# Kernel optimization log

Hardware: AMD Instinct MI355X
Metric: run time of the kernel (lower is better)

The kernel has to match this reference:

```python
import jax, jax.numpy as jnp
import numpy as np
import math

D, DK, DV = 1024, 128, 128
B, S = 4, 2048

def setup_inputs() -> dict:
    key = jax.random.key(0)
    k1, k2, k3, k4 = jax.random.split(key, 4)
    # xavier_normal std = sqrt(2/(fan_in+fan_out))
    std_qk = math.sqrt(2.0 / (D + DK))
    std_v = math.sqrt(2.0 / (D + DV))
    return {
        "X": jax.random.normal(k1, (B, S, D), dtype=jnp.float32),
        "W_q": jax.random.normal(k2, (D, DK), dtype=jnp.float32) * std_qk,
        "W_k": jax.random.normal(k3, (D, DK), dtype=jnp.float32) * std_qk,
        "W_v": jax.random.normal(k4, (D, DV), dtype=jnp.float32) * std_v,
    }

def reference(X, W_q, W_k, W_v):
    # Q,K,V projections: [B,S,D] @ [D,dk] -> [B,S,dk]
    Q = X @ W_q
    K = X @ W_k
    V = X @ W_v
    scale = 1.0 / math.sqrt(DK)
    # NOTE: original torch code calls A.masked_fill(...) without assigning the
    # result, so the causal mask is never actually applied. We replicate the
    # executed math: unmasked scaled dot-product attention.
    A = jnp.einsum("bqd,bkd->bqk", Q, K) * scale  # [B,S,S]
    A = jax.nn.softmax(A, axis=2)
    return jnp.einsum("bqk,bkv->bqv", A, V)  # [B,S,DV]
```

## Files before the change

kernel.cpp:

```cpp
#include <hip/hip_runtime.h>
#include <stdint.h>
#include <math.h>


typedef __attribute__((ext_vector_type(4))) float  f32x4;
typedef __attribute__((ext_vector_type(4))) short  s16x4;
typedef __attribute__((ext_vector_type(8))) short  s16x8;
typedef __attribute__((ext_vector_type(4))) float  fl4;

#define MFMA16(a,b,c) __builtin_amdgcn_mfma_f32_16x16x16bf16_1k(a,b,c,0,0,0)
#define MFMA32(a,b,c) __builtin_amdgcn_mfma_f32_16x16x32_bf16(a,b,c,0,0,0)

__device__ __forceinline__ short f2bf(float f){
  uint32_t u = __builtin_bit_cast(uint32_t, f);
  u = (u + 0x7FFFu + ((u >> 16) & 1u)) >> 16;
  return (short)u;
}

#define S_LEN   2048
#define D_IN    1024
#define D_HEAD  128
#define NROWS   8192
#define NSPLIT  8
#define KVB     64
#define KVPER   (S_LEN / NSPLIT)
#define NT      (KVPER / KVB)
#define QBLK    128

#define WT_OFF  0u
#define Q_OFF   786432u
#define K_OFF   (786432u + 2097152u)
#define V_OFF   (786432u + 2u*2097152u)
#define OP_OFF  (786432u + 3u*2097152u)
#define ML_OFF  (OP_OFF + 33554432u)

#define LOG2E   1.4426950408889634f
#define DEFER_TH 11.541560327111708f

__global__ __launch_bounds__(256) void wt3_kernel(
    const float* __restrict__ Wq, const float* __restrict__ Wk,
    const float* __restrict__ Wv, short* __restrict__ Wt){
  int i = blockIdx.x * 256 + threadIdx.x;
  int m = i >> 17;
  int r = i & 131071;
  int n = r >> 10;
  int k = r & 1023;
  const float* W = (m == 0) ? Wq : (m == 1 ? Wk : Wv);
  float v = W[k * D_HEAD + n];
  if (m == 0) v *= 0.08838834764831845f * LOG2E;
  Wt[i] = f2bf(v);
}

__global__ __launch_bounds__(256) void proj_kernel(
    const float* __restrict__ X, const short* __restrict__ Wt,
    short* __restrict__ Qo, short* __restrict__ Ko, short* __restrict__ Vt){
  const int mt  = blockIdx.x;
  const int mat = blockIdx.y;
  const short* Wm = Wt + mat * 131072;

  __shared__ short Xs[64][72];
  __shared__ short Ws[128][72];

  const int tid  = threadIdx.x;
  const int lane = tid & 63;
  const int wid  = tid >> 6;
  const int wm   = (wid >> 1) * 32;
  const int wn   = (wid & 1) * 64;
  const int lr   = lane & 15;
  const int lg8  = (lane >> 4) * 8;

  const f32x4 zero4 = {0.f, 0.f, 0.f, 0.f};
  f32x4 acc[2][4];
  #pragma unroll
  for (int mf = 0; mf < 2; mf++)
    #pragma unroll
    for (int n = 0; n < 4; n++) acc[mf][n] = zero4;

  const int xr = tid >> 2, xc = (tid & 3) * 16;
  const int wr = tid >> 1, wc = (tid & 1) * 32;

  const float* xsrc0 = X + (size_t)(mt * 64 + xr) * D_IN + xc;
  const short* wsrc0 = Wm + (size_t)wr * D_IN + wc;

  fl4   xA[4];
  s16x8 wR[4];

  #pragma unroll
  for (int j = 0; j < 4; j++){
    xA[j] = *(const fl4*)(xsrc0 + 4 * j);
    wR[j] = *(const s16x8*)(wsrc0 + 8 * j);
  }

  #pragma unroll 1
  for (int kt = 0; kt < D_IN; kt += 64){
    {
      s16x8 v0, v1;
      #pragma unroll
      for (int j = 0; j < 4; j++){
        v0[j] = f2bf(xA[0][j]); v0[j+4] = f2bf(xA[1][j]);
        v1[j] = f2bf(xA[2][j]); v1[j+4] = f2bf(xA[3][j]);
      }
      *(s16x8*)&Xs[xr][xc]     = v0;
      *(s16x8*)&Xs[xr][xc + 8] = v1;
      #pragma unroll
      for (int j = 0; j < 4; j++) *(s16x8*)&Ws[wr][wc + 8*j] = wR[j];
    }
    __syncthreads();

    if (kt + 64 < D_IN){
      #pragma unroll
      for (int j = 0; j < 4; j++){
        xA[j] = *(const fl4*)(xsrc0 + kt + 64 + 4*j);
        wR[j] = *(const s16x8*)(wsrc0 + kt + 64 + 8*j);
      }
    }

    #pragma unroll
    for (int kc = 0; kc < 64; kc += 32){
      s16x8 af[2];
      #pragma unroll
      for (int mf = 0; mf < 2; mf++)
        af[mf] = *(const s16x8*)&Xs[wm + mf*16 + lr][kc + lg8];
      #pragma unroll
      for (int n = 0; n < 4; n++){
        s16x8 bf = *(const s16x8*)&Ws[wn + n*16 + lr][kc + lg8];
        #pragma unroll
        for (int mf = 0; mf < 2; mf++)
          acc[mf][n] = MFMA32(af[mf], bf, acc[mf][n]);
      }
    }
    __syncthreads();
  }

  const int lg4 = (lane >> 4) * 4;
  if (mat < 2){
    short* dst = (mat == 0) ? Qo : Ko;
    #pragma unroll
    for (int mf = 0; mf < 2; mf++)
      #pragma unroll
      for (int n = 0; n < 4; n++){
        int col = wn + n*16 + lr;
        #pragma unroll
        for (int r = 0; r < 4; r++){
          int row = mt*64 + wm + mf*16 + lg4 + r;
          dst[(size_t)row * D_HEAD + col] = f2bf(acc[mf][n][r]);
        }
      }
  } else {
    const int b  = (mt * 64) >> 11;
    const int s0 = (mt * 64) & 2047;
    #pragma unroll
    for (int mf = 0; mf < 2; mf++)
      #pragma unroll
      for (int n = 0; n < 4; n++){
        int dv = wn + n*16 + lr;
        int s  = s0 + wm + mf*16 + lg4;
        s16x4 v;
        #pragma unroll
        for (int r = 0; r < 4; r++) v[r] = f2bf(acc[mf][n][r]);
        *(s16x4*)&Vt[((size_t)b * D_HEAD + dv) * S_LEN + s] = v;
      }
  }
}

__global__ __launch_bounds__(256) void flash_kernel(
    const short* __restrict__ Q, const short* __restrict__ K,
    const short* __restrict__ Vt, float* __restrict__ Opart,
    float* __restrict__ MLpart){
  const int sp = blockIdx.x;
  const int qt = blockIdx.y;
  const int b  = blockIdx.z;

  __shared__ short Ks[KVB][136];
  __shared__ short Vs[128][72];

  const int tid  = threadIdx.x;
  const int lane = tid & 63;
  const int w    = tid >> 6;
  const int lr   = lane & 15;
  const int lg   = lane >> 4;

  const int qrow0 = qt * QBLK + w * 32 + lr;
  const short* Qr = Q + (size_t)(b * S_LEN + qrow0) * D_HEAD + 8 * lg;
  s16x8 qf[2][4];
  #pragma unroll
  for (int qi = 0; qi < 2; qi++)
    #pragma unroll
    for (int c = 0; c < 4; c++)
      qf[qi][c] = *(const s16x8*)(Qr + qi * 16 * D_HEAD + c * 32);

  const f32x4 zero4 = {0.f, 0.f, 0.f, 0.f};
  f32x4 o[2][8];
  #pragma unroll
  for (int qi = 0; qi < 2; qi++)
    #pragma unroll
    for (int t = 0; t < 8; t++) o[qi][t] = zero4;
  float m_run[2] = {-INFINITY, -INFINITY};
  float l_run[2] = {0.0f, 0.0f};

  const short* Kb = K  + (size_t)b * S_LEN * D_HEAD;
  const short* Vb = Vt + (size_t)b * D_HEAD * S_LEN;
  const int kr = tid >> 2, kc = (tid & 3) * 32;
  const int vr = tid >> 1, vc = (tid & 1) * 32;

  s16x8 kR[4], vR[4];
  const int kv_beg = sp * KVPER;

  {
    const short* ks = Kb + (size_t)(kv_beg + kr) * D_HEAD + kc;
    const short* vs = Vb + (size_t)vr * S_LEN + kv_beg + vc;
    #pragma unroll
    for (int j = 0; j < 4; j++){
      kR[j] = *(const s16x8*)(ks + 8*j);
      vR[j] = *(const s16x8*)(vs + 8*j);
    }
  }
  #pragma unroll
  for (int j = 0; j < 4; j++){
    *(s16x8*)&Ks[kr][kc + 8*j] = kR[j];
    *(s16x8*)&Vs[vr][vc + 8*j] = vR[j];
  }
  __syncthreads();

  #pragma unroll 1
  for (int it = 0; it < NT; ++it){
    if (it + 1 < NT){
      int kv0 = kv_beg + (it + 1) * KVB;
      const short* ks = Kb + (size_t)(kv0 + kr) * D_HEAD + kc;
      const short* vs = Vb + (size_t)vr * S_LEN + kv0 + vc;
      #pragma unroll
      for (int j = 0; j < 4; j++){
        kR[j] = *(const s16x8*)(ks + 8*j);
        vR[j] = *(const s16x8*)(vs + 8*j);
      }
    }

    f32x4 sa[2][4];
    #pragma unroll
    for (int qi = 0; qi < 2; qi++)
      #pragma unroll
      for (int t = 0; t < 4; t++) sa[qi][t] = zero4;
    __builtin_amdgcn_s_setprio(1);
    #pragma unroll
    for (int c = 0; c < 4; c++){
      #pragma unroll
      for (int t = 0; t < 4; t++){
        s16x8 ka = *(const s16x8*)&Ks[t*16 + lr][c*32 + 8*lg];
        sa[0][t] = MFMA32(ka, qf[0][c], sa[0][t]);
        sa[1][t] = MFMA32(ka, qf[1][c], sa[1][t]);
      }
    }
    __builtin_amdgcn_s_setprio(0);

    s16x4 pb[2][4];
    #pragma unroll
    for (int qi = 0; qi < 2; qi++){
      float mx = -INFINITY;
      #pragma unroll
      for (int t = 0; t < 4; t++)
        #pragma unroll
        for (int r = 0; r < 4; r++) mx = fmaxf(mx, sa[qi][t][r]);
      mx = fmaxf(mx, __shfl_xor(mx, 16));
      mx = fmaxf(mx, __shfl_xor(mx, 32));
      if (!__all(mx <= m_run[qi] + DEFER_TH)){
        float m_new = fmaxf(m_run[qi], mx);
        float alpha = exp2f(m_run[qi] - m_new);
        l_run[qi] *= alpha;
        #pragma unroll
        for (int t = 0; t < 8; t++) o[qi][t] *= alpha;
        m_run[qi] = m_new;
      }
      float lsum = 0.0f;
      #pragma unroll
      for (int t = 0; t < 4; t++)
        #pragma unroll
        for (int r = 0; r < 4; r++){
          float e = exp2f(sa[qi][t][r] - m_run[qi]);
          pb[qi][t][r] = f2bf(e);
          lsum += e;
        }
      lsum += __shfl_xor(lsum, 16);
      lsum += __shfl_xor(lsum, 32);
      l_run[qi] += lsum;
    }

    __builtin_amdgcn_s_setprio(1);
    #pragma unroll
    for (int dt = 0; dt < 8; dt++){
      #pragma unroll
      for (int t = 0; t < 4; t++){
        s16x4 va = *(const s16x4*)&Vs[dt*16 + lr][t*16 + 4*lg];
        o[0][dt] = MFMA16(va, pb[0][t], o[0][dt]);
        o[1][dt] = MFMA16(va, pb[1][t], o[1][dt]);
      }
    }
    __builtin_amdgcn_s_setprio(0);

    if (it + 1 < NT){
      __syncthreads();
      #pragma unroll
      for (int j = 0; j < 4; j++){
        *(s16x8*)&Ks[kr][kc + 8*j] = kR[j];
        *(s16x8*)&Vs[vr][vc + 8*j] = vR[j];
      }
      __syncthreads();
    }
  }

  const int lg4 = lg * 4;
  #pragma unroll
  for (int qi = 0; qi < 2; qi++){
    const size_t grow = (size_t)b * S_LEN + qrow0 + qi * 16;
    float* Op = Opart + ((size_t)sp * NROWS + grow) * D_HEAD + lg4;
    #pragma unroll
    for (int dt = 0; dt < 8; dt++)
      *(f32x4*)(Op + dt * 16) = o[qi][dt];
    if (lg == 0){
      float* ml = MLpart + ((size_t)sp * NROWS + grow) * 2;
      ml[0] = m_run[qi]; ml[1] = l_run[qi];
    }
  }
}

__global__ __launch_bounds__(256) void merge_kernel(
    const float* __restrict__ Opart, const float* __restrict__ MLpart,
    float* __restrict__ out){
  int idx = blockIdx.x * 256 + threadIdx.x;
  int row = idx >> 7;
  float m[NSPLIT], l[NSPLIT];
  float M = -INFINITY;
  #pragma unroll
  for (int s = 0; s < NSPLIT; s++){
    m[s] = MLpart[((size_t)s * NROWS + row) * 2 + 0];
    l[s] = MLpart[((size_t)s * NROWS + row) * 2 + 1];
    M = fmaxf(M, m[s]);
  }
  float L = 0.f, val = 0.f;
  #pragma unroll
  for (int s = 0; s < NSPLIT; s++){
    float e = exp2f(m[s] - M);
    L   += l[s] * e;
    val += Opart[(size_t)s * NROWS * D_HEAD + idx] * e;
  }
  out[idx] = val / L;
}

extern "C" void kernel_launch(void* const* d_in, const int* in_sizes, int n_in,
                              void* d_out, int out_size, void* d_ws, size_t ws_size,
                              hipStream_t stream){
  const float* X  = (const float*)d_in[0];
  const float* Wq = (const float*)d_in[1];
  const float* Wk = (const float*)d_in[2];
  const float* Wv = (const float*)d_in[3];
  char* ws = (char*)d_ws;
  short* Wt = (short*)(ws + WT_OFF);
  short* Qp = (short*)(ws + Q_OFF);
  short* Kp = (short*)(ws + K_OFF);
  short* Vt = (short*)(ws + V_OFF);
  float* Op = (float*)(ws + OP_OFF);
  float* Ml = (float*)(ws + ML_OFF);
  float* out = (float*)d_out;

  wt3_kernel  <<<dim3(1536),           dim3(256), 0, stream>>>(Wq, Wk, Wv, Wt);
  proj_kernel <<<dim3(128, 3),         dim3(256), 0, stream>>>(X, Wt, Qp, Kp, Vt);
  flash_kernel<<<dim3(NSPLIT, 16, 4),  dim3(256), 0, stream>>>(Qp, Kp, Vt, Op, Ml);
  merge_kernel<<<dim3(4096),           dim3(256), 0, stream>>>(Op, Ml, out);
}
```

Baseline: 141.1 us.

## Halve flash query tile to 64 rows, one 16-row fragment per wave

Each wave of the flash kernel now handles 16 query rows instead of 32, so the query block drops to 64 and the grid doubles along the query axis. The per-thread accumulator, score and query registers are halved, and launch bounds request 4 blocks per CU to raise occupancy and the number of resident blocks. In exchange every K/V tile loaded into shared memory is reused by half as many query rows, which doubles global and LDS traffic for K and V.

```diff
diff --git a/kernel.cpp b/kernel.cpp
--- a/kernel.cpp
+++ b/kernel.cpp
@@ -25,7 +25,7 @@
 #define KVB     64
 #define KVPER   (S_LEN / NSPLIT)
 #define NT      (KVPER / KVB)
-#define QBLK    128
+#define QBLK    64
 
 #define WT_OFF  0u
 #define Q_OFF   786432u
@@ -163,7 +163,7 @@
   }
 }
 
-__global__ __launch_bounds__(256) void flash_kernel(
+__global__ __launch_bounds__(256, 4) void flash_kernel(
     const short* __restrict__ Q, const short* __restrict__ K,
     const short* __restrict__ Vt, float* __restrict__ Opart,
     float* __restrict__ MLpart){
@@ -180,23 +180,17 @@
   const int lr   = lane & 15;
   const int lg   = lane >> 4;
 
-  const int qrow0 = qt * QBLK + w * 32 + lr;
-  const short* Qr = Q + (size_t)(b * S_LEN + qrow0) * D_HEAD + 8 * lg;
-  s16x8 qf[2][4];
-  #pragma unroll
-  for (int qi = 0; qi < 2; qi++)
-    #pragma unroll
-    for (int c = 0; c < 4; c++)
-      qf[qi][c] = *(const s16x8*)(Qr + qi * 16 * D_HEAD + c * 32);
+  const int qrow = qt * QBLK + w * 16 + lr;
+  const short* Qr = Q + (size_t)(b * S_LEN + qrow) * D_HEAD + 8 * lg;
+  s16x8 qf[4];
+  #pragma unroll
+  for (int c = 0; c < 4; c++) qf[c] = *(const s16x8*)(Qr + c * 32);
 
   const f32x4 zero4 = {0.f, 0.f, 0.f, 0.f};
-  f32x4 o[2][8];
-  #pragma unroll
-  for (int qi = 0; qi < 2; qi++)
-    #pragma unroll
-    for (int t = 0; t < 8; t++) o[qi][t] = zero4;
-  float m_run[2] = {-INFINITY, -INFINITY};
-  float l_run[2] = {0.0f, 0.0f};
+  f32x4 o[8];
+  #pragma unroll
+  for (int t = 0; t < 8; t++) o[t] = zero4;
+  float m_run = -INFINITY, l_run = 0.0f;
 
   const short* Kb = K  + (size_t)b * S_LEN * D_HEAD;
   const short* Vb = Vt + (size_t)b * D_HEAD * S_LEN;
@@ -235,54 +229,48 @@
       }
     }
 
-    f32x4 sa[2][4];
-    #pragma unroll
-    for (int qi = 0; qi < 2; qi++)
-      #pragma unroll
-      for (int t = 0; t < 4; t++) sa[qi][t] = zero4;
+    f32x4 sa[4];
+    #pragma unroll
+    for (int t = 0; t < 4; t++) sa[t] = zero4;
     __builtin_amdgcn_s_setprio(1);
     #pragma unroll
     for (int c = 0; c < 4; c++){
       #pragma unroll
       for (int t = 0; t < 4; t++){
         s16x8 ka = *(const s16x8*)&Ks[t*16 + lr][c*32 + 8*lg];
-        sa[0][t] = MFMA32(ka, qf[0][c], sa[0][t]);
-        sa[1][t] = MFMA32(ka, qf[1][c], sa[1][t]);
+        sa[t] = MFMA32(ka, qf[c], sa[t]);
       }
     }
     __builtin_amdgcn_s_setprio(0);
 
-    s16x4 pb[2][4];
-    #pragma unroll
-    for (int qi = 0; qi < 2; qi++){
-      float mx = -INFINITY;
-      #pragma unroll
-      for (int t = 0; t < 4; t++)
-        #pragma unroll
-        for (int r = 0; r < 4; r++) mx = fmaxf(mx, sa[qi][t][r]);
-      mx = fmaxf(mx, __shfl_xor(mx, 16));
-      mx = fmaxf(mx, __shfl_xor(mx, 32));
-      if (!__all(mx <= m_run[qi] + DEFER_TH)){
-        float m_new = fmaxf(m_run[qi], mx);
-        float alpha = exp2f(m_run[qi] - m_new);
-        l_run[qi] *= alpha;
-        #pragma unroll
-        for (int t = 0; t < 8; t++) o[qi][t] *= alpha;
-        m_run[qi] = m_new;
-      }
-      float lsum = 0.0f;
-      #pragma unroll
-      for (int t = 0; t < 4; t++)
-        #pragma unroll
-        for (int r = 0; r < 4; r++){
-          float e = exp2f(sa[qi][t][r] - m_run[qi]);
-          pb[qi][t][r] = f2bf(e);
-          lsum += e;
-        }
-      lsum += __shfl_xor(lsum, 16);
-      lsum += __shfl_xor(lsum, 32);
-      l_run[qi] += lsum;
-    }
+    float mx = -INFINITY;
+    #pragma unroll
+    for (int t = 0; t < 4; t++)
+      #pragma unroll
+      for (int r = 0; r < 4; r++) mx = fmaxf(mx, sa[t][r]);
+    mx = fmaxf(mx, __shfl_xor(mx, 16));
+    mx = fmaxf(mx, __shfl_xor(mx, 32));
+    if (!__all(mx <= m_run + DEFER_TH)){
+      float m_new = fmaxf(m_run, mx);
+      float alpha = exp2f(m_run - m_new);
+      l_run *= alpha;
+      #pragma unroll
+      for (int t = 0; t < 8; t++) o[t] *= alpha;
+      m_run = m_new;
+    }
+    s16x4 pb[4];
+    float lsum = 0.0f;
+    #pragma unroll
+    for (int t = 0; t < 4; t++)
+      #pragma unroll
+      for (int r = 0; r < 4; r++){
+        float e = exp2f(sa[t][r] - m_run);
+        pb[t][r] = f2bf(e);
+        lsum += e;
+      }
+    lsum += __shfl_xor(lsum, 16);
+    lsum += __shfl_xor(lsum, 32);
+    l_run += lsum;
 
     __builtin_amdgcn_s_setprio(1);
     #pragma unroll
@@ -290,8 +278,7 @@
       #pragma unroll
       for (int t = 0; t < 4; t++){
         s16x4 va = *(const s16x4*)&Vs[dt*16 + lr][t*16 + 4*lg];
-        o[0][dt] = MFMA16(va, pb[0][t], o[0][dt]);
-        o[1][dt] = MFMA16(va, pb[1][t], o[1][dt]);
+        o[dt] = MFMA16(va, pb[t], o[dt]);
       }
     }
     __builtin_amdgcn_s_setprio(0);
@@ -308,17 +295,14 @@
   }
 
   const int lg4 = lg * 4;
-  #pragma unroll
-  for (int qi = 0; qi < 2; qi++){
-    const size_t grow = (size_t)b * S_LEN + qrow0 + qi * 16;
-    float* Op = Opart + ((size_t)sp * NROWS + grow) * D_HEAD + lg4;
-    #pragma unroll
-    for (int dt = 0; dt < 8; dt++)
-      *(f32x4*)(Op + dt * 16) = o[qi][dt];
-    if (lg == 0){
-      float* ml = MLpart + ((size_t)sp * NROWS + grow) * 2;
-      ml[0] = m_run[qi]; ml[1] = l_run[qi];
-    }
+  const size_t grow = (size_t)b * S_LEN + qrow;
+  float* Op = Opart + ((size_t)sp * NROWS + grow) * D_HEAD + lg4;
+  #pragma unroll
+  for (int dt = 0; dt < 8; dt++)
+    *(f32x4*)(Op + dt * 16) = o[dt];
+  if (lg == 0){
+    float* ml = MLpart + ((size_t)sp * NROWS + grow) * 2;
+    ml[0] = m_run; ml[1] = l_run;
   }
 }
 
@@ -363,6 +347,6 @@
 
   wt3_kernel  <<<dim3(1536),           dim3(256), 0, stream>>>(Wq, Wk, Wv, Wt);
   proj_kernel <<<dim3(128, 3),         dim3(256), 0, stream>>>(X, Wt, Qp, Kp, Vt);
-  flash_kernel<<<dim3(NSPLIT, 16, 4),  dim3(256), 0, stream>>>(Qp, Kp, Vt, Op, Ml);
+  flash_kernel<<<dim3(NSPLIT, 32, 4),  dim3(256), 0, stream>>>(Qp, Kp, Vt, Op, Ml);
   merge_kernel<<<dim3(4096),           dim3(256), 0, stream>>>(Op, Ml, out);
 }
```

Result: faster. 129.0 us (-8.6%).
